# Optimization experiments

Measured on AMD Instinct MI355X. Metric: run time of the kernel, lower is better.

The kernel has to match this reference:

```python
import jax, jax.numpy as jnp
import numpy as np
import math
from jax import lax

IN_C = 512
OUT_C = 512
K = 3
GROUPS = 1
EXP_NITER = 5
MAXC = max(IN_C, OUT_C)
PAD_A = int(math.ceil((K - 1) / 2))  # left/top pad
PAD_B = int(math.floor((K - 1) / 2))  # right/bottom pad


def pad_fct(x):
    # ConstantPad2d((ceil, floor, ceil, floor), 0) on last two dims
    return jnp.pad(x, ((0, 0), (0, 0), (PAD_A, PAD_B), (PAD_A, PAD_B)))


def fast_matrix_conv(m1, m2, groups=1):
    # m1: (m, n, k1, k2); m2: (nb, m//groups, l1, l2)
    # composes two conv kernels: result (nb, n, k+l-1, k+l-1)
    m, n, k1, k2 = m1.shape
    nb, mb, l1, l2 = m2.shape
    x = jnp.transpose(m1, (1, 0, 2, 3))          # (n, m, k1, k2) -> batch=n, chan=m
    w = jnp.flip(m2, (-2, -1))                   # true convolution via flip
    r = lax.conv_general_dilated(
        x, w, window_strides=(1, 1),
        padding=[(l1 - 1, l1 - 1), (l2 - 1, l2 - 1)],
        dimension_numbers=("NCHW", "OIHW", "NCHW"),
        feature_group_count=groups,
    )                                            # (n, nb, k1+l1-1, k2+l2-1)
    return jnp.transpose(r, (1, 0, 2, 3))


def identity_kernel():
    gic = MAXC // GROUPS
    eye = jnp.eye(gic, dtype=jnp.float32)[:, :, None, None]     # (gic, gic, 1, 1)
    eye = jnp.tile(eye[None], (GROUPS, 1, 1, 1, 1)).reshape(MAXC, gic, 1, 1)
    return pad_fct(eye)                                          # (MAXC, gic, K, K)


def setup_inputs() -> dict:
    key = jax.random.key(0)
    kernel = jax.random.normal(key, (MAXC, MAXC // GROUPS, K, K), dtype=jnp.float32) * 0.05
    return {"kernel": kernel}


def reference(kernel):
    kg = kernel + identity_kernel()
    ki = kernel
    for i in range(2, EXP_NITER + 1):
        ki = fast_matrix_conv(ki, kernel, GROUPS) / float(i)
        kg = pad_fct(kg) + ki
    g = GROUPS
    kh, kw = kg.shape[-2], kg.shape[-1]
    kg = kg.reshape(g, MAXC // g, MAXC // g, kh, kw)
    kg = kg[:, : OUT_C // g, : IN_C // g, :, :]
    return kg.reshape(OUT_C, IN_C // g, kh, kw)
```

## Files before the change

kernel.cpp:

```cpp
#include <hip/hip_runtime.h>
#include <stdint.h>

#define C 512
#define C2 262144

typedef __attribute__((ext_vector_type(8))) short bf16x8;
typedef __attribute__((ext_vector_type(4))) float f32x4;

__device__ __forceinline__ unsigned short f2bf(float f) {
    union { float f; uint32_t u; } v; v.f = f;
    uint32_t u = v.u;
    u += 0x7fffu + ((u >> 16) & 1u);
    return (unsigned short)(u >> 16);
}
__device__ __forceinline__ float bf2f(unsigned short h) {
    union { uint32_t u; float f; } v; v.u = ((uint32_t)h) << 16;
    return v.f;
}

#define GL2LDS16(g, l) __builtin_amdgcn_global_load_lds( \
    (const __attribute__((address_space(1))) void*)(g),  \
    (__attribute__((address_space(3))) void*)(l), 16, 0, 0)

__device__ __forceinline__ bf16x8 ldsr16(const char* p) {
    bf16x8 r;
    asm volatile("ds_read_b128 %0, %1"
                 : "=v"(r)
                 : "v"((__attribute__((address_space(3))) const void*)p));
    return r;
}

__device__ __forceinline__ int nth_valid(int mask, int n) {
    int pq = 0;
    while (true) {
        if (mask & 1) { if (n == 0) return pq; --n; }
        mask >>= 1; ++pq;
    }
}

__global__ void k_transform(const float* __restrict__ K,
                            unsigned short* __restrict__ Kt,
                            unsigned short* __restrict__ KtT,
                            float* __restrict__ Ktf) {
    int t = blockIdx.x * 256 + threadIdx.x;
    int a = t >> 9, b = t & 511;
#pragma unroll
    for (int j = 0; j < 9; ++j) {
        float v = K[(size_t)t * 9 + j];
        unsigned short h = f2bf(v);
        Kt[(size_t)j * C2 + t] = h;
        KtT[(size_t)j * C2 + (size_t)b * C + a] = h;
        Ktf[(size_t)j * C2 + (size_t)b * C + a] = v;
    }
}

__global__ void k_sched(int* __restrict__ sched, int splits) {
    __shared__ int hist[4][10];
    __shared__ int base[4][10];
    const int tid = threadIdx.x;
    if (tid < 40) ((int*)hist)[tid] = 0;
    if (tid < 4) sched[tid] = 0;
    __syncthreads();
    const int offs[5] = {0, 25, 74, 155, 276};
    const int Loff[4] = {0, 140, 504, 1008};
    int step = -1, yx = 0, V = 0, nch = 1, bsz = 0, rem = 0;
    if (tid < 276) {
#pragma unroll
        for (int s = 0; s < 4; ++s)
            if (tid >= offs[s] && tid < offs[s + 1]) { step = s; yx = tid - offs[s]; }
        const int s_out = 5 + 2 * step, s_in = s_out - 2;
        const int y = yx / s_out, x = yx % s_out;
        int vy = 0, vx = 0;
#pragma unroll
        for (int p = 0; p < 3; ++p) {
            if (y - p >= 0 && y - p < s_in) ++vy;
            if (x - p >= 0 && x - p < s_in) ++vx;
        }
        V = vy * vx;
        const int sp = (splits >> (4 * step)) & 15;
        nch = (V >= 6 && sp > 1) ? sp : 1;
        bsz = V / nch; rem = V % nch;
        for (int j = 0; j < nch; ++j)
            atomicAdd(&hist[step][bsz + (j < rem ? 1 : 0)], 1);
    }
    __syncthreads();
    if (tid < 4) {
        int a = 0;
        for (int v = 9; v >= 1; --v) { base[tid][v] = a; a += hist[tid][v]; hist[tid][v] = 0; }
    }
    __syncthreads();
    if (tid < 276) {
        int* L = sched + 4 + Loff[step];
        for (int j = 0; j < nch; ++j) {
            const int sz = bsz + (j < rem ? 1 : 0);
            const int idx = atomicAdd(&hist[step][sz], 1);
            int* w = L + (base[step][sz] + idx) * 4;
            w[0] = yx * 16 + 0 + j; w[1] = yx * 16 + 4 + j;
            w[2] = yx * 16 + 8 + j; w[3] = yx * 16 + 12 + j;
        }
    }
}

__global__ __launch_bounds__(256) void k_merge(
    unsigned short* __restrict__ Out, const unsigned short* __restrict__ P1,
    const unsigned short* __restrict__ P2, const int* __restrict__ list,
    int has3)
{
    const int code = list[blockIdx.x];
    if ((code & 3) != 1) return;
    const int quad = (code >> 2) & 3, yx = code >> 4;
    const int i0 = (quad & 1) * 256, o0 = (quad >> 1) * 256;
    const int t = threadIdx.x;
    const int r = blockIdx.y * 16 + (t >> 4);
    const int c = (t & 15) * 16;
    const size_t base = ((size_t)yx * C + i0 + r) * C + o0 + c;
    bf16x8* po = (bf16x8*)(Out + base);
    const bf16x8* p1 = (const bf16x8*)(P1 + base);
    const bf16x8* p2 = (const bf16x8*)(P2 + base);
#pragma unroll
    for (int h = 0; h < 2; ++h) {
        bf16x8 a = po[h], b = p1[h];
#pragma unroll
        for (int k = 0; k < 8; ++k) {
            float s = bf2f((unsigned short)a[k]) + bf2f((unsigned short)b[k]);
            a[k] = (short)f2bf(s);
        }
        if (has3) {
            bf16x8 cvec = p2[h];
#pragma unroll
            for (int k = 0; k < 8; ++k)
                a[k] = (short)f2bf(bf2f((unsigned short)a[k]) + bf2f((unsigned short)cvec[k]));
        }
        po[h] = a;
    }
}

__global__ __launch_bounds__(512, 2) void k_gemm(
    const unsigned short* __restrict__ A,
    const unsigned short* __restrict__ Bm,
    unsigned short* __restrict__ Out,
    int s_in, int s_out, float alpha,
    int* __restrict__ ctr, const int* __restrict__ list, int n_items,
    unsigned short* __restrict__ Pb1, unsigned short* __restrict__ Pb2,
    int split)
{
    __shared__ __align__(16) char lds[131072];
    __shared__ int s_item;

    const int tid = threadIdx.x;
    const int lane = tid & 63, wid = tid >> 6;
    const int wr = wid >> 2, wc = wid & 3;
    const int l15 = lane & 15, lhi = lane >> 4;

    const int soff = (tid >> 3) * 1024 + ((((tid & 7) ^ ((tid >> 3) & 7))) << 4);
    const int t16 = tid * 16;

    const int coff0 = ((lhi ^ (l15 & 7)) << 4);
    const int coff1 = (((4 + lhi) ^ (l15 & 7)) << 4);
    const int aoff = wr * 16384 + l15 * 128;
    const int boff = 32768 + wc * 8192 + l15 * 128;

    const char* Abase = (const char*)A;
    const char* Bbase = (const char*)Bm;

#define STAGE4(SRC, DSTOFF) { \
        const char* s_ = (SRC) + soff; \
        GL2LDS16(s_,          lds + (DSTOFF) + t16); \
        GL2LDS16(s_ + 65536,  lds + (DSTOFF) + 8192 + t16); \
        GL2LDS16(s_ + 131072, lds + (DSTOFF) + 16384 + t16); \
        GL2LDS16(s_ + 196608, lds + (DSTOFF) + 24576 + t16); \
    }

    for (;;) {
        __syncthreads();
        if (tid == 0) s_item = atomicAdd(ctr, 1);
        __syncthreads();
        const int itm = s_item;
        if (itm >= n_items) break;
        const int code = list[itm];
        const int j = code & 3;
        const int quad = (code >> 2) & 3;
        const int yx = code >> 4;
        const int i0 = (quad & 1) * 256, o0 = (quad >> 1) * 256;
        const int y = yx / s_out, x = yx % s_out;

        int mask = 0, V = 0;
        for (int pq = 0; pq < 9; ++pq) {
            int u = y - pq / 3, v = x - pq % 3;
            if (u >= 0 && u < s_in && v >= 0 && v < s_in) { mask |= 1 << pq; ++V; }
        }
        const int nch = (split > 1 && V >= 6) ? split : 1;
        const int bsz = V / nch, rem = V % nch;
        const int cnt = bsz + (j < rem ? 1 : 0);
        const int c0 = j * bsz + (j < rem ? j : rem);
        unsigned short* ob = (j == 0) ? Out : ((j == 1) ? Pb1 : Pb2);

        auto slabA = [&](int pq) {
            int u = y - pq / 3, v = x - pq % 3;
            return Abase + ((size_t)(u * s_in + v) * C + i0) * (size_t)(C * 2);
        };
        auto slabB = [&](int pq) {
            return Bbase + ((size_t)pq * C + o0) * (size_t)(C * 2);
        };
        const int pq0 = nth_valid(mask, c0);
        const char* slA = slabA(pq0);
        const char* slB = slabB(pq0);
        const char* nsA = slA;
        const char* nsB = slB;
        if (cnt > 1) { int p1 = nth_valid(mask, c0 + 1); nsA = slabA(p1); nsB = slabB(p1); }

        f32x4 acc[8][4] = {};
        bf16x8 bBa[4], bBb[4];
        bf16x8 aE[4], aO[4];

        STAGE4(slA, 0)
        STAGE4(slB, 32768)
        asm volatile("s_waitcnt vmcnt(0)" ::: "memory");
        __builtin_amdgcn_s_barrier();
        __builtin_amdgcn_sched_barrier(0);
#pragma unroll
        for (int n = 0; n < 4; ++n)
            bBa[n] = ldsr16(lds + boff + n * 2048 + coff0);
#pragma unroll
        for (int mi = 0; mi < 4; ++mi)
            aE[mi] = ldsr16(lds + aoff + mi * 2048 + coff0);

        const int NI = 8 * cnt;
        for (int it = 0; it < NI; ++it) {
            const int itl = it & 7;
            const bool lastq = (itl == 7);
            const bool dummy = lastq && (((it >> 3) + 1) >= cnt);
            const char* sAe = lastq ? nsA : slA;
            const char* sBe = lastq ? nsB : slB;
            const int kb = lastq ? 0 : (itl + 1) * 128;
            const char* cur = lds + (it & 1) * 65536;
            const char* nxt = lds + ((it & 1) ^ 1) * 65536;

#define PHASE(PH) { \
        constexpr int mh_ = (PH) & 1; \
        constexpr int mhn_ = ((PH) + 1) & 1; \
        constexpr int parn_ = ((PH) == 3) ? 0 : (((PH) + 1) >> 1); \
        const int coffn_ = parn_ ? coff1 : coff0; \
         \
        { \
            const char* ab_ = ((PH) == 3) ? nxt : cur; \
            _Pragma("unroll") for (int mi = 0; mi < 4; ++mi) { \
                bf16x8 t0 = ldsr16(ab_ + aoff + mhn_ * 8192 + mi * 2048 + coffn_); \
                if constexpr (((PH) & 1) == 0) aO[mi] = t0; else aE[mi] = t0; \
            } \
        } \
         \
        if constexpr ((PH) == 1) { \
            _Pragma("unroll") for (int n = 0; n < 4; ++n) \
                bBb[n] = ldsr16(cur + boff + n * 2048 + coff1); \
        } \
        if constexpr ((PH) == 3) { \
            _Pragma("unroll") for (int n = 0; n < 4; ++n) \
                bBa[n] = ldsr16(nxt + boff + n * 2048 + coff0); \
        } \
         \
        if constexpr ((PH) == 0) { if (!dummy) STAGE4(sAe + kb, ((it & 1) ^ 1) * 65536) } \
        if constexpr ((PH) == 1) { if (!dummy) STAGE4(sBe + kb, ((it & 1) ^ 1) * 65536 + 32768) } \
        if constexpr ((PH) == 1 || (PH) == 3) { \
            asm volatile("s_waitcnt lgkmcnt(8)" ::: "memory"); \
        } else { \
            asm volatile("s_waitcnt lgkmcnt(4)" ::: "memory"); \
        } \
        __builtin_amdgcn_sched_barrier(0); \
        __builtin_amdgcn_s_setprio(1); \
        _Pragma("unroll") for (int mi = 0; mi < 4; ++mi) \
        _Pragma("unroll") for (int n = 0; n < 4; ++n) { \
            if constexpr ((PH) == 0) \
                acc[mi][n] = __builtin_amdgcn_mfma_f32_16x16x32_bf16(aE[mi], bBa[n], acc[mi][n], 0, 0, 0); \
            else if constexpr ((PH) == 1) \
                acc[4 + mi][n] = __builtin_amdgcn_mfma_f32_16x16x32_bf16(aO[mi], bBa[n], acc[4 + mi][n], 0, 0, 0); \
            else if constexpr ((PH) == 2) \
                acc[mi][n] = __builtin_amdgcn_mfma_f32_16x16x32_bf16(aE[mi], bBb[n], acc[mi][n], 0, 0, 0); \
            else \
                acc[4 + mi][n] = __builtin_amdgcn_mfma_f32_16x16x32_bf16(aO[mi], bBb[n], acc[4 + mi][n], 0, 0, 0); \
        } \
        __builtin_amdgcn_s_setprio(0); \
        if constexpr ((PH) == 2) { \
            asm volatile("s_waitcnt vmcnt(0)" ::: "memory"); \
            __builtin_amdgcn_s_barrier(); \
            __builtin_amdgcn_sched_barrier(0); \
        } \
        if constexpr ((PH) == 3) { \
            __builtin_amdgcn_s_barrier(); \
            __builtin_amdgcn_sched_barrier(0); \
        } \
    }

            PHASE(0) PHASE(1) PHASE(2) PHASE(3)
#undef PHASE

            if (lastq) {
                slA = nsA; slB = nsB;
                int vn = (it >> 3) + 2;
                if (vn < cnt) {
                    int pqn = nth_valid(mask, c0 + vn);
                    nsA = slabA(pqn); nsB = slabB(pqn);
                }
            }
        }
        asm volatile("s_waitcnt lgkmcnt(0)" ::: "memory");
        __builtin_amdgcn_sched_barrier(0);

#pragma unroll
        for (int M = 0; M < 8; ++M) {
#pragma unroll
            for (int r = 0; r < 4; ++r) {
                const int irow = i0 + wr * 128 + M * 16 + lhi * 4 + r;
                unsigned short* op = ob + ((size_t)yx * C + irow) * C
                                   + o0 + wc * 64 + l15;
#pragma unroll
                for (int n = 0; n < 4; ++n)
                    op[n * 16] = f2bf(acc[M][n][r] * alpha);
            }
        }
    }
#undef STAGE4
    asm volatile("s_waitcnt vmcnt(0)" ::: "memory");
}

__global__ __launch_bounds__(256) void k_final(
    const unsigned short* __restrict__ Ka, int sa, int ofa,
    const unsigned short* __restrict__ Kb, int sb, int ofb,
    const float* __restrict__ Ktf, float* __restrict__ kg, int init)
{
    __shared__ float L[64 * 121];
    const int i = blockIdx.x;
    const int o0 = blockIdx.y * 64;
    const int tid = threadIdx.x, lane = tid & 63, wid = tid >> 6;

    for (int idx = tid; idx < 64 * 121; idx += 256) L[idx] = 0.f;
    __syncthreads();

    const int sa2 = sa * sa;
    for (int yxv = wid; yxv < sa2; yxv += 4) {
        float v = bf2f(Ka[((size_t)yxv * C + i) * C + o0 + lane]);
        int yy = yxv / sa + ofa, xx = yxv % sa + ofa;
        L[lane * 121 + yy * 11 + xx] += v;
    }
    __syncthreads();
    const int sb2 = sb * sb;
    for (int yxv = wid; yxv < sb2; yxv += 4) {
        float v = bf2f(Kb[((size_t)yxv * C + i) * C + o0 + lane]);
        int yy = yxv / sb + ofb, xx = yxv % sb + ofb;
        L[lane * 121 + yy * 11 + xx] += v;
    }
    __syncthreads();
    if (init) {
        for (int j = wid; j < 9; j += 4) {
            float v = Ktf[(size_t)j * C2 + (size_t)i * C + o0 + lane];
            if (j == 4 && (o0 + lane) == i) v += 1.0f;
            L[lane * 121 + (j / 3 + 4) * 11 + (j % 3 + 4)] += v;
        }
    }
    __syncthreads();
    if (init) {
        for (int idx = tid; idx < 64 * 121; idx += 256) {
            int ol = idx / 121, w = idx - ol * 121;
            kg[((size_t)(o0 + ol) * C + i) * 121 + w] = L[idx];
        }
    } else {
        for (int idx = tid; idx < 64 * 121; idx += 256) {
            int ol = idx / 121, w = idx - ol * 121;
            kg[((size_t)(o0 + ol) * C + i) * 121 + w] += L[idx];
        }
    }
}

__global__ __launch_bounds__(256) void k_final4(
    const unsigned short* __restrict__ K2, const unsigned short* __restrict__ K3,
    const unsigned short* __restrict__ K4, const unsigned short* __restrict__ K5,
    const float* __restrict__ Ktf, float* __restrict__ kg)
{
    __shared__ float L[64 * 121];
    const int i = blockIdx.x;
    const int o0 = blockIdx.y * 64;
    const int tid = threadIdx.x, lane = tid & 63, wid = tid >> 6;

    for (int idx = tid; idx < 64 * 121; idx += 256) L[idx] = 0.f;
    __syncthreads();

#define ADDSRC(SRC, S, OFS) { \
        const int total_ = (S) * (S) * 8; \
        for (int idx = tid; idx < total_; idx += 256) { \
            const int yxv = idx >> 3, l3 = idx & 7; \
            bf16x8 v = *(const bf16x8*)&(SRC)[((size_t)yxv * C + i) * C + o0 + l3 * 8]; \
            const int w = (yxv / (S) + (OFS)) * 11 + yxv % (S) + (OFS); \
            _Pragma("unroll") for (int k = 0; k < 8; ++k) \
                L[(l3 * 8 + k) * 121 + w] += bf2f((unsigned short)v[k]); \
        } \
        __syncthreads(); \
    }
    ADDSRC(K2, 5, 3) ADDSRC(K3, 7, 2) ADDSRC(K4, 9, 1) ADDSRC(K5, 11, 0)
#undef ADDSRC

    for (int j = wid; j < 9; j += 4) {
        float v = Ktf[(size_t)j * C2 + (size_t)i * C + o0 + lane];
        if (j == 4 && (o0 + lane) == i) v += 1.0f;
        L[lane * 121 + (j / 3 + 4) * 11 + (j % 3 + 4)] += v;
    }
    __syncthreads();
    for (int idx = tid; idx < 64 * 121; idx += 256) {
        int ol = idx / 121, w = idx - ol * 121;
        kg[((size_t)(o0 + ol) * C + i) * 121 + w] = L[idx];
    }
}

extern "C" void kernel_launch(void* const* d_in, const int* in_sizes, int n_in,
                              void* d_out, int out_size, void* d_ws, size_t ws_size,
                              hipStream_t stream) {
    const float* K = (const float*)d_in[0];
    float* kg = (float*)d_out;
    char* ws = (char*)d_ws;

    unsigned short* Kt  = (unsigned short*)(ws);
    unsigned short* KtT = (unsigned short*)(ws + (size_t)4718592);
    float*          Ktf = (float*)         (ws + (size_t)9437184);

    const bool big = (ws_size >= (size_t)163585616);

    if (big) {
        unsigned short* Ki2 = (unsigned short*)(ws + (size_t)18874368);
        unsigned short* Ki3 = (unsigned short*)(ws + (size_t)31981568);
        unsigned short* Ki4 = (unsigned short*)(ws + (size_t)57671680);
        unsigned short* Ki5 = (unsigned short*)(ws + (size_t)100139008);
        int* sch = (int*)(ws + (size_t)163577856);
        int* lst = sch + 4;
        unsigned short* PbA = Ki5;
        unsigned short* PbB = Ki4;

        k_transform<<<1024, 256, 0, stream>>>(K, Kt, KtT, Ktf);
        k_sched<<<1, 320, 0, stream>>>(sch, 0x1233);
        k_gemm<<<256, 512, 0, stream>>>(KtT, Kt, Ki2, 3, 5, 0.5f,
                                        sch + 0, lst + 0, 140, PbA, PbB, 3);
        k_merge<<<dim3(140, 16), 256, 0, stream>>>(Ki2, PbA, PbB, lst + 0, 1);
        k_gemm<<<256, 512, 0, stream>>>(Ki2, Kt, Ki3, 5, 7, 1.0f / 3.0f,
                                        sch + 1, lst + 140, 364, PbA, PbB, 3);
        k_merge<<<dim3(364, 16), 256, 0, stream>>>(Ki3, PbA, PbB, lst + 140, 1);
        k_gemm<<<256, 512, 0, stream>>>(Ki3, Kt, Ki4, 7, 9, 0.25f,
                                        sch + 2, lst + 504, 504, PbA, PbA, 2);
        k_merge<<<dim3(504, 16), 256, 0, stream>>>(Ki4, PbA, PbA, lst + 504, 0);
        k_gemm<<<256, 512, 0, stream>>>(Ki4, Kt, Ki5, 9, 11, 0.2f,
                                        sch + 3, lst + 1008, 484, PbA, PbA, 1);
        k_final4<<<dim3(512, 8), 256, 0, stream>>>(Ki2, Ki3, Ki4, Ki5, Ktf, kg);
    } else {
        unsigned short* P1 = (unsigned short*)(ws + (size_t)18874368);
        unsigned short* P2 = (unsigned short*)(ws + (size_t)61341696);
        int* sch = (int*)(ws + (size_t)124780544);
        int* lst = sch + 4;
        unsigned short* Pb2 = P2;
        unsigned short* Pb3 = P1 + 6553600;

        k_transform<<<1024, 256, 0, stream>>>(K, Kt, KtT, Ktf);
        k_sched<<<1, 320, 0, stream>>>(sch, 0x1122);
        k_gemm<<<256, 512, 0, stream>>>(KtT, Kt, P1, 3, 5, 0.5f,
                                        sch + 0, lst + 0, 140, Pb2, Pb2, 2);
        k_merge<<<dim3(140, 16), 256, 0, stream>>>(P1, Pb2, Pb2, lst + 0, 0);
        k_gemm<<<256, 512, 0, stream>>>(P1, Kt, P2, 5, 7, 1.0f / 3.0f,
                                        sch + 1, lst + 140, 364, Pb3, Pb3, 2);
        k_merge<<<dim3(364, 16), 256, 0, stream>>>(P2, Pb3, Pb3, lst + 140, 0);
        k_final<<<dim3(512, 8), 256, 0, stream>>>(P1, 5, 3, P2, 7, 2, Ktf, kg, 1);
        k_gemm<<<256, 512, 0, stream>>>(P2, Kt, P1, 7, 9, 0.25f,
                                        sch + 2, lst + 504, 324, Pb2, Pb2, 1);
        k_gemm<<<256, 512, 0, stream>>>(P1, Kt, P2, 9, 11, 0.2f,
                                        sch + 3, lst + 1008, 484, Pb2, Pb2, 1);
        k_final<<<dim3(512, 8), 256, 0, stream>>>(P1, 9, 1, P2, 11, 0, Ktf, kg, 0);
    }
}
```

Before: 515.1 us.

## Shrink GEMM tiles to 128x256 with 256-thread blocks and smaller double buffer

Each GEMM work item shrinks from a 256x256 quadrant handled by 512 threads to a 128x256 tile handled by 256 threads. The schedule list now stores one entry per position, and each entry expands to 8 tiles. The LDS footprint drops from 128 KB to 48 KB, K-steps shrink to 64, the pipeline is restructured into two half-steps with double buffering, and the merge kernel is adapted to full-row entries. The goal is better occupancy and load balance across CUs. The cost is less data reuse per tile and more barriers per unit of work.

```diff
diff --git a/kernel.cpp b/kernel.cpp
--- a/kernel.cpp
+++ b/kernel.cpp
@@ -62,7 +62,7 @@
     if (tid < 4) sched[tid] = 0;
     __syncthreads();
     const int offs[5] = {0, 25, 74, 155, 276};
-    const int Loff[4] = {0, 140, 504, 1008};
+    const int Loff[4] = {0, 35, 126, 252};
     int step = -1, yx = 0, V = 0, nch = 1, bsz = 0, rem = 0;
     if (tid < 276) {
 #pragma unroll
@@ -94,9 +94,7 @@
         for (int j = 0; j < nch; ++j) {
             const int sz = bsz + (j < rem ? 1 : 0);
             const int idx = atomicAdd(&hist[step][sz], 1);
-            int* w = L + (base[step][sz] + idx) * 4;
-            w[0] = yx * 16 + 0 + j; w[1] = yx * 16 + 4 + j;
-            w[2] = yx * 16 + 8 + j; w[3] = yx * 16 + 12 + j;
+            L[base[step][sz] + idx] = yx * 4 + j;
         }
     }
 }
@@ -108,23 +106,20 @@
 {
     const int code = list[blockIdx.x];
     if ((code & 3) != 1) return;
-    const int quad = (code >> 2) & 3, yx = code >> 4;
-    const int i0 = (quad & 1) * 256, o0 = (quad >> 1) * 256;
+    const int yx = code >> 2;
     const int t = threadIdx.x;
     const int r = blockIdx.y * 16 + (t >> 4);
-    const int c = (t & 15) * 16;
-    const size_t base = ((size_t)yx * C + i0 + r) * C + o0 + c;
+    const int cb = (t & 15) * 32;
+    const size_t base = ((size_t)yx * C + r) * C + cb;
     bf16x8* po = (bf16x8*)(Out + base);
     const bf16x8* p1 = (const bf16x8*)(P1 + base);
     const bf16x8* p2 = (const bf16x8*)(P2 + base);
 #pragma unroll
-    for (int h = 0; h < 2; ++h) {
+    for (int h = 0; h < 4; ++h) {
         bf16x8 a = po[h], b = p1[h];
 #pragma unroll
-        for (int k = 0; k < 8; ++k) {
-            float s = bf2f((unsigned short)a[k]) + bf2f((unsigned short)b[k]);
-            a[k] = (short)f2bf(s);
-        }
+        for (int k = 0; k < 8; ++k)
+            a[k] = (short)f2bf(bf2f((unsigned short)a[k]) + bf2f((unsigned short)b[k]));
         if (has3) {
             bf16x8 cvec = p2[h];
 #pragma unroll
@@ -135,7 +130,7 @@
     }
 }
 
-__global__ __launch_bounds__(512, 2) void k_gemm(
+__global__ __launch_bounds__(256, 2) void k_gemm(
     const unsigned short* __restrict__ A,
     const unsigned short* __restrict__ Bm,
     unsigned short* __restrict__ Out,
@@ -144,32 +139,22 @@
     unsigned short* __restrict__ Pb1, unsigned short* __restrict__ Pb2,
     int split)
 {
-    __shared__ __align__(16) char lds[131072];
+    __shared__ __align__(16) char lds[49152];
     __shared__ int s_item;
 
     const int tid = threadIdx.x;
-    const int lane = tid & 63, wid = tid >> 6;
-    const int wr = wid >> 2, wc = wid & 3;
+    const int lane = tid & 63, wc = tid >> 6;
     const int l15 = lane & 15, lhi = lane >> 4;
 
-    const int soff = (tid >> 3) * 1024 + ((((tid & 7) ^ ((tid >> 3) & 7))) << 4);
+    const int soff = (tid >> 2) * 1024 + ((((tid & 3) ^ ((tid >> 2) & 3))) << 4);
     const int t16 = tid * 16;
 
-    const int coff0 = ((lhi ^ (l15 & 7)) << 4);
-    const int coff1 = (((4 + lhi) ^ (l15 & 7)) << 4);
-    const int aoff = wr * 16384 + l15 * 128;
-    const int boff = 32768 + wc * 8192 + l15 * 128;
+    const int fo = ((lhi ^ (l15 & 3)) << 4);
+    const int aoff = l15 * 64 + fo;
+    const int boff = (wc * 64 + l15) * 64 + fo;
 
     const char* Abase = (const char*)A;
     const char* Bbase = (const char*)Bm;
-
-#define STAGE4(SRC, DSTOFF) { \
-        const char* s_ = (SRC) + soff; \
-        GL2LDS16(s_,          lds + (DSTOFF) + t16); \
-        GL2LDS16(s_ + 65536,  lds + (DSTOFF) + 8192 + t16); \
-        GL2LDS16(s_ + 131072, lds + (DSTOFF) + 16384 + t16); \
-        GL2LDS16(s_ + 196608, lds + (DSTOFF) + 24576 + t16); \
-    }
 
     for (;;) {
         __syncthreads();
@@ -177,11 +162,11 @@
         __syncthreads();
         const int itm = s_item;
         if (itm >= n_items) break;
-        const int code = list[itm];
-        const int j = code & 3;
-        const int quad = (code >> 2) & 3;
-        const int yx = code >> 4;
-        const int i0 = (quad & 1) * 256, o0 = (quad >> 1) * 256;
+        const int entry = list[itm >> 3];
+        const int tile = itm & 7;
+        const int j = entry & 3;
+        const int yx = entry >> 2;
+        const int i0 = (tile & 3) * 128, o0 = (tile >> 2) * 256;
         const int y = yx / s_out, x = yx % s_out;
 
         int mask = 0, V = 0;
@@ -213,96 +198,77 @@
         bf16x8 bBa[4], bBb[4];
         bf16x8 aE[4], aO[4];
 
-        STAGE4(slA, 0)
-        STAGE4(slB, 32768)
+#define STAGE_AB(SA, SB, BUF) { \
+        const char* a_ = (SA) + soff; \
+        GL2LDS16(a_,         lds + (BUF) + t16); \
+        GL2LDS16(a_ + 65536, lds + (BUF) + 4096 + t16); \
+        const char* b_ = (SB) + soff; \
+        GL2LDS16(b_,          lds + (BUF) + 8192 + t16); \
+        GL2LDS16(b_ + 65536,  lds + (BUF) + 12288 + t16); \
+        GL2LDS16(b_ + 131072, lds + (BUF) + 16384 + t16); \
+        GL2LDS16(b_ + 196608, lds + (BUF) + 20480 + t16); \
+    }
+
+        STAGE_AB(slA, slB, 0)
         asm volatile("s_waitcnt vmcnt(0)" ::: "memory");
         __builtin_amdgcn_s_barrier();
         __builtin_amdgcn_sched_barrier(0);
 #pragma unroll
         for (int n = 0; n < 4; ++n)
-            bBa[n] = ldsr16(lds + boff + n * 2048 + coff0);
+            bBa[n] = ldsr16(lds + 8192 + n * 1024 + boff);
 #pragma unroll
         for (int mi = 0; mi < 4; ++mi)
-            aE[mi] = ldsr16(lds + aoff + mi * 2048 + coff0);
-
-        const int NI = 8 * cnt;
-        for (int it = 0; it < NI; ++it) {
-            const int itl = it & 7;
-            const bool lastq = (itl == 7);
-            const bool dummy = lastq && (((it >> 3) + 1) >= cnt);
-            const char* sAe = lastq ? nsA : slA;
-            const char* sBe = lastq ? nsB : slB;
-            const int kb = lastq ? 0 : (itl + 1) * 128;
-            const char* cur = lds + (it & 1) * 65536;
-            const char* nxt = lds + ((it & 1) ^ 1) * 65536;
-
-#define PHASE(PH) { \
-        constexpr int mh_ = (PH) & 1; \
-        constexpr int mhn_ = ((PH) + 1) & 1; \
-        constexpr int parn_ = ((PH) == 3) ? 0 : (((PH) + 1) >> 1); \
-        const int coffn_ = parn_ ? coff1 : coff0; \
+            aE[mi] = ldsr16(lds + mi * 1024 + aoff);
+
+#define SUBITER(CURB, NXTB, BBS, BBO, IT_) { \
+        const int itl_ = (IT_) & 15; \
+        const bool lastq_ = (itl_ == 15); \
+        const bool dummy_ = lastq_ && (((((IT_)) >> 4) + 1) >= cnt); \
+        const char* sA_ = lastq_ ? nsA : slA; \
+        const char* sB_ = lastq_ ? nsB : slB; \
+        const int kb_ = lastq_ ? 0 : (itl_ + 1) * 64; \
          \
-        { \
-            const char* ab_ = ((PH) == 3) ? nxt : cur; \
-            _Pragma("unroll") for (int mi = 0; mi < 4; ++mi) { \
-                bf16x8 t0 = ldsr16(ab_ + aoff + mhn_ * 8192 + mi * 2048 + coffn_); \
-                if constexpr (((PH) & 1) == 0) aO[mi] = t0; else aE[mi] = t0; \
-            } \
-        } \
-         \
-        if constexpr ((PH) == 1) { \
-            _Pragma("unroll") for (int n = 0; n < 4; ++n) \
-                bBb[n] = ldsr16(cur + boff + n * 2048 + coff1); \
-        } \
-        if constexpr ((PH) == 3) { \
-            _Pragma("unroll") for (int n = 0; n < 4; ++n) \
-                bBa[n] = ldsr16(nxt + boff + n * 2048 + coff0); \
-        } \
-         \
-        if constexpr ((PH) == 0) { if (!dummy) STAGE4(sAe + kb, ((it & 1) ^ 1) * 65536) } \
-        if constexpr ((PH) == 1) { if (!dummy) STAGE4(sBe + kb, ((it & 1) ^ 1) * 65536 + 32768) } \
-        if constexpr ((PH) == 1 || (PH) == 3) { \
-            asm volatile("s_waitcnt lgkmcnt(8)" ::: "memory"); \
-        } else { \
-            asm volatile("s_waitcnt lgkmcnt(4)" ::: "memory"); \
-        } \
+        _Pragma("unroll") for (int mi = 0; mi < 4; ++mi) \
+            aO[mi] = ldsr16(lds + (CURB) + (mi + 4) * 1024 + aoff); \
+        if (!dummy_) STAGE_AB(sA_ + kb_, sB_ + kb_, NXTB) \
+        asm volatile("s_waitcnt lgkmcnt(4)" ::: "memory"); \
         __builtin_amdgcn_sched_barrier(0); \
         __builtin_amdgcn_s_setprio(1); \
         _Pragma("unroll") for (int mi = 0; mi < 4; ++mi) \
-        _Pragma("unroll") for (int n = 0; n < 4; ++n) { \
-            if constexpr ((PH) == 0) \
-                acc[mi][n] = __builtin_amdgcn_mfma_f32_16x16x32_bf16(aE[mi], bBa[n], acc[mi][n], 0, 0, 0); \
-            else if constexpr ((PH) == 1) \
-                acc[4 + mi][n] = __builtin_amdgcn_mfma_f32_16x16x32_bf16(aO[mi], bBa[n], acc[4 + mi][n], 0, 0, 0); \
-            else if constexpr ((PH) == 2) \
-                acc[mi][n] = __builtin_amdgcn_mfma_f32_16x16x32_bf16(aE[mi], bBb[n], acc[mi][n], 0, 0, 0); \
-            else \
-                acc[4 + mi][n] = __builtin_amdgcn_mfma_f32_16x16x32_bf16(aO[mi], bBb[n], acc[4 + mi][n], 0, 0, 0); \
+        _Pragma("unroll") for (int n = 0; n < 4; ++n) \
+            acc[mi][n] = __builtin_amdgcn_mfma_f32_16x16x32_bf16(aE[mi], BBS[n], acc[mi][n], 0, 0, 0); \
+        __builtin_amdgcn_s_setprio(0); \
+        asm volatile("s_waitcnt vmcnt(0)" ::: "memory"); \
+        __builtin_amdgcn_s_barrier(); \
+        __builtin_amdgcn_sched_barrier(0); \
+         \
+        _Pragma("unroll") for (int mi = 0; mi < 4; ++mi) \
+            aE[mi] = ldsr16(lds + (NXTB) + mi * 1024 + aoff); \
+        _Pragma("unroll") for (int n = 0; n < 4; ++n) \
+            BBO[n] = ldsr16(lds + (NXTB) + 8192 + n * 1024 + boff); \
+        asm volatile("s_waitcnt lgkmcnt(8)" ::: "memory"); \
+        __builtin_amdgcn_sched_barrier(0); \
+        __builtin_amdgcn_s_setprio(1); \
+        _Pragma("unroll") for (int mi = 0; mi < 4; ++mi) \
+        _Pragma("unroll") for (int n = 0; n < 4; ++n) \
+            acc[4 + mi][n] = __builtin_amdgcn_mfma_f32_16x16x32_bf16(aO[mi], BBS[n], acc[4 + mi][n], 0, 0, 0); \
+        __builtin_amdgcn_s_setprio(0); \
+        __builtin_amdgcn_s_barrier(); \
+        __builtin_amdgcn_sched_barrier(0); \
+        if (lastq_) { \
+            slA = nsA; slB = nsB; \
+            int vn_ = (((IT_)) >> 4) + 2; \
+            if (vn_ < cnt) { int pqn_ = nth_valid(mask, c0 + vn_); nsA = slabA(pqn_); nsB = slabB(pqn_); } \
         } \
-        __builtin_amdgcn_s_setprio(0); \
-        if constexpr ((PH) == 2) { \
-            asm volatile("s_waitcnt vmcnt(0)" ::: "memory"); \
-            __builtin_amdgcn_s_barrier(); \
-            __builtin_amdgcn_sched_barrier(0); \
-        } \
-        if constexpr ((PH) == 3) { \
-            __builtin_amdgcn_s_barrier(); \
-            __builtin_amdgcn_sched_barrier(0); \
-        } \
-    }
-
-            PHASE(0) PHASE(1) PHASE(2) PHASE(3)
-#undef PHASE
-
-            if (lastq) {
-                slA = nsA; slB = nsB;
-                int vn = (it >> 3) + 2;
-                if (vn < cnt) {
-                    int pqn = nth_valid(mask, c0 + vn);
-                    nsA = slabA(pqn); nsB = slabB(pqn);
-                }
-            }
-        }
+    }
+
+        const int NI = 16 * cnt;
+        for (int it2 = 0; it2 < NI; it2 += 2) {
+            SUBITER(0,     24576, bBa, bBb, it2)
+            SUBITER(24576, 0,     bBb, bBa, it2 + 1)
+        }
+#undef SUBITER
+#undef STAGE_AB
         asm volatile("s_waitcnt lgkmcnt(0)" ::: "memory");
         __builtin_amdgcn_sched_barrier(0);
 
@@ -310,7 +276,7 @@
         for (int M = 0; M < 8; ++M) {
 #pragma unroll
             for (int r = 0; r < 4; ++r) {
-                const int irow = i0 + wr * 128 + M * 16 + lhi * 4 + r;
+                const int irow = i0 + M * 16 + lhi * 4 + r;
                 unsigned short* op = ob + ((size_t)yx * C + irow) * C
                                    + o0 + wc * 64 + l15;
 #pragma unroll
@@ -319,7 +285,6 @@
             }
         }
     }
-#undef STAGE4
     asm volatile("s_waitcnt vmcnt(0)" ::: "memory");
 }
 
@@ -435,17 +400,17 @@
 
         k_transform<<<1024, 256, 0, stream>>>(K, Kt, KtT, Ktf);
         k_sched<<<1, 320, 0, stream>>>(sch, 0x1233);
-        k_gemm<<<256, 512, 0, stream>>>(KtT, Kt, Ki2, 3, 5, 0.5f,
-                                        sch + 0, lst + 0, 140, PbA, PbB, 3);
-        k_merge<<<dim3(140, 16), 256, 0, stream>>>(Ki2, PbA, PbB, lst + 0, 1);
-        k_gemm<<<256, 512, 0, stream>>>(Ki2, Kt, Ki3, 5, 7, 1.0f / 3.0f,
-                                        sch + 1, lst + 140, 364, PbA, PbB, 3);
-        k_merge<<<dim3(364, 16), 256, 0, stream>>>(Ki3, PbA, PbB, lst + 140, 1);
-        k_gemm<<<256, 512, 0, stream>>>(Ki3, Kt, Ki4, 7, 9, 0.25f,
-                                        sch + 2, lst + 504, 504, PbA, PbA, 2);
-        k_merge<<<dim3(504, 16), 256, 0, stream>>>(Ki4, PbA, PbA, lst + 504, 0);
-        k_gemm<<<256, 512, 0, stream>>>(Ki4, Kt, Ki5, 9, 11, 0.2f,
-                                        sch + 3, lst + 1008, 484, PbA, PbA, 1);
+        k_gemm<<<512, 256, 0, stream>>>(KtT, Kt, Ki2, 3, 5, 0.5f,
+                                        sch + 0, lst + 0, 280, PbA, PbB, 3);
+        k_merge<<<dim3(35, 32), 256, 0, stream>>>(Ki2, PbA, PbB, lst + 0, 1);
+        k_gemm<<<512, 256, 0, stream>>>(Ki2, Kt, Ki3, 5, 7, 1.0f / 3.0f,
+                                        sch + 1, lst + 35, 728, PbA, PbB, 3);
+        k_merge<<<dim3(91, 32), 256, 0, stream>>>(Ki3, PbA, PbB, lst + 35, 1);
+        k_gemm<<<512, 256, 0, stream>>>(Ki3, Kt, Ki4, 7, 9, 0.25f,
+                                        sch + 2, lst + 126, 1008, PbA, PbA, 2);
+        k_merge<<<dim3(126, 32), 256, 0, stream>>>(Ki4, PbA, PbA, lst + 126, 0);
+        k_gemm<<<512, 256, 0, stream>>>(Ki4, Kt, Ki5, 9, 11, 0.2f,
+                                        sch + 3, lst + 252, 968, PbA, PbA, 1);
         k_final4<<<dim3(512, 8), 256, 0, stream>>>(Ki2, Ki3, Ki4, Ki5, Ktf, kg);
     } else {
         unsigned short* P1 = (unsigned short*)(ws + (size_t)18874368);
@@ -457,17 +422,17 @@
 
         k_transform<<<1024, 256, 0, stream>>>(K, Kt, KtT, Ktf);
         k_sched<<<1, 320, 0, stream>>>(sch, 0x1122);
-        k_gemm<<<256, 512, 0, stream>>>(KtT, Kt, P1, 3, 5, 0.5f,
-                                        sch + 0, lst + 0, 140, Pb2, Pb2, 2);
-        k_merge<<<dim3(140, 16), 256, 0, stream>>>(P1, Pb2, Pb2, lst + 0, 0);
-        k_gemm<<<256, 512, 0, stream>>>(P1, Kt, P2, 5, 7, 1.0f / 3.0f,
-                                        sch + 1, lst + 140, 364, Pb3, Pb3, 2);
-        k_merge<<<dim3(364, 16), 256, 0, stream>>>(P2, Pb3, Pb3, lst + 140, 0);
+        k_gemm<<<512, 256, 0, stream>>>(KtT, Kt, P1, 3, 5, 0.5f,
+                                        sch + 0, lst + 0, 240, Pb2, Pb2, 2);
+        k_merge<<<dim3(30, 32), 256, 0, stream>>>(P1, Pb2, Pb2, lst + 0, 0);
+        k_gemm<<<512, 256, 0, stream>>>(P1, Kt, P2, 5, 7, 1.0f / 3.0f,
+                                        sch + 1, lst + 35, 560, Pb3, Pb3, 2);
+        k_merge<<<dim3(70, 32), 256, 0, stream>>>(P2, Pb3, Pb3, lst + 35, 0);
         k_final<<<dim3(512, 8), 256, 0, stream>>>(P1, 5, 3, P2, 7, 2, Ktf, kg, 1);
-        k_gemm<<<256, 512, 0, stream>>>(P2, Kt, P1, 7, 9, 0.25f,
-                                        sch + 2, lst + 504, 324, Pb2, Pb2, 1);
-        k_gemm<<<256, 512, 0, stream>>>(P1, Kt, P2, 9, 11, 0.2f,
-                                        sch + 3, lst + 1008, 484, Pb2, Pb2, 1);
+        k_gemm<<<512, 256, 0, stream>>>(P2, Kt, P1, 7, 9, 0.25f,
+                                        sch + 2, lst + 126, 648, Pb2, Pb2, 1);
+        k_gemm<<<512, 256, 0, stream>>>(P1, Kt, P2, 9, 11, 0.2f,
+                                        sch + 3, lst + 252, 968, Pb2, Pb2, 1);
         k_final<<<dim3(512, 8), 256, 0, stream>>>(P1, 9, 1, P2, 11, 0, Ktf, kg, 0);
     }
 }
```

After: 602.1 us. +16.9%, slower.
